# Optimization experiments

Measured on AMD Instinct MI355X. Metric: run time of the kernel, lower is better.

Reference implementation:

```python
import jax, jax.numpy as jnp
import numpy as np

D = 200            # embedding_dim == GRU hidden size
N_LABELS = 28000   # MeSH label count (graph nodes)
VOCAB = 50000
B = 4
T_AB = 384         # abstract length
T_TI = 64          # title length
N_EDGES = 224000   # ~8 edges per label node


def reverse_padded(x, lengths):
    # reverse the first lengths[b] timesteps of each padded sequence
    T = x.shape[1]
    t = jnp.arange(T)
    idx = jnp.where(t[None, :] < lengths[:, None], lengths[:, None] - 1 - t[None, :], t[None, :])
    return jnp.take_along_axis(x, idx[:, :, None], axis=1)


def gru_dir(x, lengths, wih, whh, bih, bhh, reverse):
    # PyTorch-semantics GRU over a padded batch (packed-sequence equivalent):
    # hidden state freezes past each sequence length; padded outputs are zero.
    Bb, T, _ = x.shape
    Hh = whh.shape[1]
    if reverse:
        x = reverse_padded(x, lengths)
    gx = jnp.einsum('bti,gi->btg', x, wih) + bih   # [B,T,3H], torch gate order r,z,n

    def step(h, inp):
        g_t, t = inp
        gh = h @ whh.T + bhh
        r = jax.nn.sigmoid(g_t[:, :Hh] + gh[:, :Hh])
        z = jax.nn.sigmoid(g_t[:, Hh:2 * Hh] + gh[:, Hh:2 * Hh])
        n = jnp.tanh(g_t[:, 2 * Hh:] + r * gh[:, 2 * Hh:])
        h_new = (1.0 - z) * n + z * h
        mask = (t < lengths)[:, None]
        h = jnp.where(mask, h_new, h)
        return h, jnp.where(mask, h_new, 0.0)

    h0 = jnp.zeros((Bb, Hh), x.dtype)
    _, outs = jax.lax.scan(step, h0, (jnp.swapaxes(gx, 0, 1), jnp.arange(T)))
    outs = jnp.swapaxes(outs, 0, 1)
    if reverse:
        outs = reverse_padded(outs, lengths)
    return outs


def forward_impl(input_abstract, input_title, ab_length, title_length, edge_src, edge_dst,
                 g_node_feature, emb,
                 wih_l0f, whh_l0f, bih_l0f, bhh_l0f, wih_l0b, whh_l0b, bih_l0b, bhh_l0b,
                 wih_l1f, whh_l1f, bih_l1f, bhh_l1f, wih_l1b, whh_l1b, bih_l1b, bhh_l1b,
                 gcn_w1, gcn_b1, gcn_w2, gcn_b2, fc1_w, fc1_b, fc2_w, fc2_b):
    # --- LabelNet: two GCN layers (copy_src message + sum reduce, then Linear) ---
    def gcn_layer(feat, W, b):
        agg = jax.ops.segment_sum(feat[edge_src], edge_dst, num_segments=N_LABELS)
        return agg @ W.T + b

    h = jax.nn.relu(gcn_layer(g_node_feature, gcn_w1, gcn_b1))
    lab = gcn_layer(h, gcn_w2, gcn_b2)
    label_feature = jnp.concatenate([lab, g_node_feature], axis=1)   # [N, 2D]

    gru_params = [
        (wih_l0f, whh_l0f, bih_l0f, bhh_l0f, wih_l0b, whh_l0b, bih_l0b, bhh_l0b),
        (wih_l1f, whh_l1f, bih_l1f, bhh_l1f, wih_l1b, whh_l1b, bih_l1b, bhh_l1b),
    ]

    def branch(tokens, lengths):
        x = emb[tokens]                                              # [B,T,D]
        for (wif, whf, bif, bhf, wib, whb, bib, bhb) in gru_params:
            f = gru_dir(x, lengths, wif, whf, bif, bhf, False)
            bwd = gru_dir(x, lengths, wib, whb, bib, bhb, True)
            x = jnp.concatenate([f, bwd], axis=-1)                   # [B,T,2D]
        # doc-label cross attention: softmax over the sequence dim (dim=1).
        # Padded positions output zero vectors -> logit 0, included in softmax
        # exactly as in the original torch code.
        atten = jax.nn.softmax(jnp.einsum('btd,nd->btn', x, label_feature), axis=1)
        return jnp.einsum('btd,btn->bnd', x, atten)                  # [B,N,2D]

    feat = branch(input_title, title_length) + branch(input_abstract, ab_length)
    y = jax.nn.leaky_relu(feat @ fc1_w.T + fc1_b, negative_slope=0.2)
    y = jax.nn.leaky_relu(y @ fc2_w.T + fc2_b, negative_slope=0.2)
    return y[..., 0]                                                 # [B, N]


def setup_inputs():
    key = jax.random.key(0)
    ks = jax.random.split(key, 32)
    it = iter(range(32))
    def nk():
        return ks[next(it)]
    s = 0.05
    inp = {}
    inp['input_abstract'] = jax.random.randint(nk(), (B, T_AB), 0, VOCAB)
    inp['input_title'] = jax.random.randint(nk(), (B, T_TI), 0, VOCAB)
    inp['ab_length'] = jax.random.randint(nk(), (B,), T_AB // 2, T_AB + 1).at[0].set(T_AB)
    inp['title_length'] = jax.random.randint(nk(), (B,), T_TI // 2, T_TI + 1).at[0].set(T_TI)
    inp['edge_src'] = jax.random.randint(nk(), (N_EDGES,), 0, N_LABELS)
    inp['edge_dst'] = jax.random.randint(nk(), (N_EDGES,), 0, N_LABELS)
    inp['g_node_feature'] = jax.random.normal(nk(), (N_LABELS, D)) * s
    inp['emb'] = jax.random.normal(nk(), (VOCAB, D)) * s
    for l in range(2):
        in_dim = D if l == 0 else 2 * D
        for d in ('f', 'b'):
            inp['wih_l%d%s' % (l, d)] = jax.random.normal(nk(), (3 * D, in_dim)) * s
            inp['whh_l%d%s' % (l, d)] = jax.random.normal(nk(), (3 * D, D)) * s
            inp['bih_l%d%s' % (l, d)] = jnp.zeros((3 * D,))
            inp['bhh_l%d%s' % (l, d)] = jnp.zeros((3 * D,))
    inp['gcn_w1'] = jax.random.normal(nk(), (D, D)) * s
    inp['gcn_b1'] = jnp.zeros((D,))
    inp['gcn_w2'] = jax.random.normal(nk(), (D, D)) * s
    inp['gcn_b2'] = jnp.zeros((D,))
    inp['fc1_w'] = jax.random.normal(nk(), (D, 2 * D)) * s
    inp['fc1_b'] = jnp.zeros((D,))
    inp['fc2_w'] = jax.random.normal(nk(), (1, D)) * s
    inp['fc2_b'] = jnp.zeros((1,))
    return inp


def reference(input_abstract, input_title, ab_length, title_length, edge_src, edge_dst,
              g_node_feature, emb,
              wih_l0f, whh_l0f, bih_l0f, bhh_l0f, wih_l0b, whh_l0b, bih_l0b, bhh_l0b,
              wih_l1f, whh_l1f, bih_l1f, bhh_l1f, wih_l1b, whh_l1b, bih_l1b, bhh_l1b,
              gcn_w1, gcn_b1, gcn_w2, gcn_b2, fc1_w, fc1_b, fc2_w, fc2_b):
    return forward_impl(input_abstract, input_title, ab_length, title_length, edge_src, edge_dst,
                        g_node_feature, emb,
                        wih_l0f, whh_l0f, bih_l0f, bhh_l0f, wih_l0b, whh_l0b, bih_l0b, bhh_l0b,
                        wih_l1f, whh_l1f, bih_l1f, bhh_l1f, wih_l1b, whh_l1b, bih_l1b, bhh_l1b,
                        gcn_w1, gcn_b1, gcn_w2, gcn_b2, fc1_w, fc1_b, fc2_w, fc2_b)
```

## Files before the change

### kernel.cpp

```cpp
#include <hip/hip_runtime.h>
#include <math.h>

#define NLAB 28000
#define NEDGE 224000
#define XFS 224

typedef _Float16 f16;
typedef _Float16 f16x8 __attribute__((ext_vector_type(8)));
typedef float f32x4 __attribute__((ext_vector_type(4)));


__device__ __forceinline__ void atomAddF(float* p, float v) {
  unsafeAtomicAdd(p, v);
}

struct RecurArgs {
  const float* gx[4];
  const float* wF[4];
  const float* bh[4];
  float* out[4];
  const int* len[4];
  int Tl[4];
  int dir[4];
};

#define COMPB(V, B) ((B) == 0 ? (V).x : (B) == 1 ? (V).y : (B) == 2 ? (V).z : (V).w)


__global__ void embed_gather(const int* __restrict__ tok, const float* __restrict__ emb,
                             float* __restrict__ x, int rows) {
  int idx = blockIdx.x * blockDim.x + threadIdx.x;
  if (idx >= rows * 50) return;
  int r = idx / 50, c = idx - r * 50;
  *(float4*)&x[(size_t)r * 200 + c * 4] =
      *(const float4*)&emb[(size_t)tok[r] * 200 + c * 4];
}


__global__ void pack_whhF(const float* __restrict__ whh, f16* __restrict__ out) {
  int e = blockIdx.x * 256 + threadIdx.x;
  if (e >= 40 * 7 * 512) return;
  int frag = e >> 9, r = e & 511;
  int l = r >> 3, j = r & 7;
  int mt = frag / 7, kt = frag - mt * 7;
  int m = mt * 16 + (l & 15);
  int k = kt * 32 + ((l >> 4) << 2) + (j & 3) + ((j >> 2) << 4);
  float v = (m < 600 && k < 200) ? whh[(size_t)m * 200 + k] : 0.f;
  f16 hi = (f16)v;
  out[e] = hi;
  out[40 * 7 * 512 + e] = (f16)((v - (float)hi) * 2048.f);
}


__global__ void gcn_gather(const float* __restrict__ feat, const int* __restrict__ src,
                           const int* __restrict__ dst, float* __restrict__ agg) {
  int wave = (int)((blockIdx.x * blockDim.x + threadIdx.x) >> 6);
  int lane = threadIdx.x & 63;
  if (wave >= NEDGE || lane >= 50) return;
  int s = src[wave], d = dst[wave];
  float4 v = *(const float4*)&feat[(size_t)s * 200 + lane * 4];
  float* p = &agg[(size_t)d * 200 + lane * 4];
  atomAddF(p + 0, v.x); atomAddF(p + 1, v.y);
  atomAddF(p + 2, v.z); atomAddF(p + 3, v.w);
}


template <int RELU, int BIAS>
__global__ __launch_bounds__(256, 2) void gemm_nt(
    const float* __restrict__ A, const float* __restrict__ Wt,
    const float* __restrict__ bias, float* __restrict__ C,
    int M, int N, int K, int ldc) {
  __shared__ float As[16][68];
  __shared__ float Bs[16][68];
  int tx = threadIdx.x & 15, ty = threadIdx.x >> 4;
  int m0 = blockIdx.y * 64, n0 = blockIdx.x * 64;
  float c[4][4] = {};
  int row = threadIdx.x >> 2;
  int kk = (threadIdx.x & 3) * 4;
  for (int k0 = 0; k0 < K; k0 += 16) {
    int gk = k0 + kk;
    float a0 = 0, a1 = 0, a2 = 0, a3 = 0;
    float b0 = 0, b1 = 0, b2 = 0, b3 = 0;
    int gm = m0 + row;
    if (gm < M) {
      if (gk + 3 < K) {
        float4 v = *(const float4*)&A[(size_t)gm * K + gk];
        a0 = v.x; a1 = v.y; a2 = v.z; a3 = v.w;
      } else {
        if (gk + 0 < K) a0 = A[(size_t)gm * K + gk + 0];
        if (gk + 1 < K) a1 = A[(size_t)gm * K + gk + 1];
        if (gk + 2 < K) a2 = A[(size_t)gm * K + gk + 2];
        if (gk + 3 < K) a3 = A[(size_t)gm * K + gk + 3];
      }
    }
    int gn = n0 + row;
    if (gn < N) {
      if (gk + 3 < K) {
        float4 v = *(const float4*)&Wt[(size_t)gn * K + gk];
        b0 = v.x; b1 = v.y; b2 = v.z; b3 = v.w;
      } else {
        if (gk + 0 < K) b0 = Wt[(size_t)gn * K + gk + 0];
        if (gk + 1 < K) b1 = Wt[(size_t)gn * K + gk + 1];
        if (gk + 2 < K) b2 = Wt[(size_t)gn * K + gk + 2];
        if (gk + 3 < K) b3 = Wt[(size_t)gn * K + gk + 3];
      }
    }
    As[kk + 0][row] = a0; As[kk + 1][row] = a1; As[kk + 2][row] = a2; As[kk + 3][row] = a3;
    Bs[kk + 0][row] = b0; Bs[kk + 1][row] = b1; Bs[kk + 2][row] = b2; Bs[kk + 3][row] = b3;
    __syncthreads();
#pragma unroll
    for (int k = 0; k < 16; k++) {
      float4 a4 = *(const float4*)&As[k][ty * 4];
      float4 b4 = *(const float4*)&Bs[k][tx * 4];
      c[0][0] = fmaf(a4.x, b4.x, c[0][0]); c[0][1] = fmaf(a4.x, b4.y, c[0][1]);
      c[0][2] = fmaf(a4.x, b4.z, c[0][2]); c[0][3] = fmaf(a4.x, b4.w, c[0][3]);
      c[1][0] = fmaf(a4.y, b4.x, c[1][0]); c[1][1] = fmaf(a4.y, b4.y, c[1][1]);
      c[1][2] = fmaf(a4.y, b4.z, c[1][2]); c[1][3] = fmaf(a4.y, b4.w, c[1][3]);
      c[2][0] = fmaf(a4.z, b4.x, c[2][0]); c[2][1] = fmaf(a4.z, b4.y, c[2][1]);
      c[2][2] = fmaf(a4.z, b4.z, c[2][2]); c[2][3] = fmaf(a4.z, b4.w, c[2][3]);
      c[3][0] = fmaf(a4.w, b4.x, c[3][0]); c[3][1] = fmaf(a4.w, b4.y, c[3][1]);
      c[3][2] = fmaf(a4.w, b4.z, c[3][2]); c[3][3] = fmaf(a4.w, b4.w, c[3][3]);
    }
    __syncthreads();
  }
#pragma unroll
  for (int i = 0; i < 4; i++) {
    int gm = m0 + ty * 4 + i;
    if (gm >= M) continue;
#pragma unroll
    for (int j = 0; j < 4; j++) {
      int gn = n0 + tx * 4 + j;
      if (gn >= N) continue;
      float v = c[i][j];
      if (BIAS) v += bias[gn];
      if (RELU) v = fmaxf(v, 0.f);
      C[(size_t)gm * ldc + gn] = v;
    }
  }
}


__global__ __launch_bounds__(512, 1) void gru_mfma(RecurArgs a) {
  int blk = blockIdx.x;
  const float* __restrict__ gx = a.gx[blk];
  const f16* __restrict__ whiP = (const f16*)a.wF[blk];
  const float* __restrict__ bh = a.bh[blk];
  float* __restrict__ outp = a.out[blk];
  const int* lenp = a.len[blk];
  int TT = a.Tl[blk];
  int bwd = a.dir[blk];
  int dirOff = bwd ? 200 : 0;

  __shared__ __align__(16) f16 wlds[16][7][512];
  __shared__ __align__(16) f16 hfrag[2][7][512];
  __shared__ float h[200][4];
  __shared__ float gh[600][4];
  __shared__ float bhs[600];
  __shared__ int lens[4];

  int tid = threadIdx.x, lane = tid & 63, w = tid >> 6;
  int l15 = lane & 15, lg = lane >> 4;

  for (int i = tid; i < 800; i += 512) ((float*)h)[i] = 0.f;
  for (int i = tid; i < 600; i += 512) bhs[i] = bh[i];
  for (int i = tid; i < 2 * 7 * 512; i += 512) ((f16*)hfrag)[i] = (f16)0.f;
  if (tid < 4) lens[tid] = lenp[tid];

#pragma unroll
  for (int i = 0; i < 2; i++)
#pragma unroll
    for (int kt = 0; kt < 7; kt++)
      *(f16x8*)&wlds[w * 2 + i][kt][lane * 8] =
          *(const f16x8*)(whiP + ((size_t)((w * 5 + i) * 7 + kt)) * 512 + lane * 8);
  __syncthreads();
  int maxlen = max(max(lens[0], lens[1]), max(lens[2], lens[3]));

  for (int s = 0; s < maxlen; s++) {
    float pgx[3][4];
    if (tid < 200) {
#pragma unroll
      for (int b = 0; b < 4; b++) {
        int Lb = lens[b];
        if (s < Lb) {
          int ta = bwd ? (Lb - 1 - s) : s;
          const float* gxr = gx + (size_t)(b * TT + ta) * 600;
          pgx[0][b] = gxr[tid];
          pgx[1][b] = gxr[200 + tid];
          pgx[2][b] = gxr[400 + tid];
        }
      }
    }
    f32x4 acc1[5], acc2[5];
#pragma unroll
    for (int i = 0; i < 5; i++) {
      acc1[i] = (f32x4){0.f, 0.f, 0.f, 0.f};
      acc2[i] = (f32x4){0.f, 0.f, 0.f, 0.f};
    }
#pragma unroll
    for (int kt = 0; kt < 7; kt++) {
      f16x8 hhi = *(const f16x8*)&hfrag[0][kt][lane * 8];
      f16x8 hlo = *(const f16x8*)&hfrag[1][kt][lane * 8];
#pragma unroll
      for (int i = 0; i < 5; i++) {
        const f16* base = whiP + ((size_t)((w * 5 + i) * 7 + kt)) * 512 + lane * 8;
        f16x8 whi = (i < 2) ? *(const f16x8*)&wlds[w * 2 + i][kt][lane * 8]
                            : *(const f16x8*)base;
        f16x8 wlo = *(const f16x8*)(base + (size_t)40 * 7 * 512);
        acc1[i] = __builtin_amdgcn_mfma_f32_16x16x32_f16(whi, hhi, acc1[i], 0, 0, 0);
        acc2[i] = __builtin_amdgcn_mfma_f32_16x16x32_f16(wlo, hhi, acc2[i], 0, 0, 0);
        acc2[i] = __builtin_amdgcn_mfma_f32_16x16x32_f16(whi, hlo, acc2[i], 0, 0, 0);
      }
    }
    if (l15 < 4) {
#pragma unroll
      for (int i = 0; i < 5; i++) {
        int mbase = (w * 5 + i) * 16 + lg * 4;
#pragma unroll
        for (int r = 0; r < 4; r++) {
          int m = mbase + r;
          if (m < 600) gh[m][l15] = acc1[i][r] + acc2[i][r] * (1.f / 2048.f);
        }
      }
    }
    __syncthreads();
    if (tid < 200) {
      int u = tid;
      float4 hold = *(const float4*)&h[u][0];
      float4 hnew = hold;
      float br = bhs[u], bz = bhs[200 + u], bn = bhs[400 + u];
#pragma unroll
      for (int b = 0; b < 4; b++) {
        int Lb = lens[b];
        if (s < Lb) {
          int ta = bwd ? (Lb - 1 - s) : s;
          float r = 1.f / (1.f + expf(-(pgx[0][b] + gh[u][b] + br)));
          float z = 1.f / (1.f + expf(-(pgx[1][b] + gh[200 + u][b] + bz)));
          float n = tanhf(pgx[2][b] + r * (gh[400 + u][b] + bn));
          float hn = (1.f - z) * n + z * COMPB(hold, b);
          if (b == 0) hnew.x = hn; else if (b == 1) hnew.y = hn;
          else if (b == 2) hnew.z = hn; else hnew.w = hn;
          outp[(size_t)(b * TT + ta) * 400 + dirOff + u] = hn;
        }
      }
      *(float4*)&h[u][0] = hnew;
      int kt = u >> 5;
      int lbase = ((u >> 2) & 3) << 4;
      int j = (u & 3) | (((u >> 4) & 1) << 2);
#pragma unroll
      for (int b = 0; b < 4; b++) {
        float hv = COMPB(hnew, b);
        f16 hi = (f16)hv;
        f16 lo = (f16)((hv - (float)hi) * 2048.f);
        hfrag[0][kt][(lbase + b) * 8 + j] = hi;
        hfrag[1][kt][(lbase + b) * 8 + j] = lo;
      }
    }
    __syncthreads();
  }
}


__global__ void cvt_lf_frags(const float* __restrict__ lab, const float* __restrict__ gnf,
                             f16* __restrict__ out) {
  int e = blockIdx.x * 256 + threadIdx.x;
  if (e >= 1752 * 13 * 512) return;
  int frag = e >> 9, r = e & 511;
  int l = r >> 3, j = r & 7;
  int nsub = frag / 13, kt = frag - nsub * 13;
  int label = nsub * 16 + (l & 15);
  int k = kt * 32 + ((l >> 4) << 2) + (j & 3) + ((j >> 2) << 4);
  float v = 0.f;
  if (label < NLAB && k < 400)
    v = (k < 200) ? lab[(size_t)label * 200 + k] : gnf[(size_t)label * 200 + k - 200];
  out[e] = (f16)v;
}

__global__ void cvt_x_frags(const float* __restrict__ x, f16* __restrict__ out, int TT) {
  int e = blockIdx.x * 256 + threadIdx.x;
  if (e >= 4 * TT * 13 * 512) return;
  int frag = e >> 9, r = e & 511;
  int l = r >> 3, j = r & 7;
  int kt = frag % 13, bt = frag / 13;
  int tt = bt % TT, b = bt / TT;
  int t = tt * 16 + (l & 15);
  int k = kt * 32 + ((l >> 4) << 2) + (j & 3) + ((j >> 2) << 4);
  float v = (k < 400) ? x[((size_t)b * TT * 16 + t) * 400 + k] : 0.f;
  out[e] = (f16)v;
}

__global__ void cvt_v_frags(const float* __restrict__ xf, f16* __restrict__ out, int KT) {
  int e = blockIdx.x * 256 + threadIdx.x;
  if (e >= 4 * KT * 13 * 2 * 512) return;
  int idx = e >> 9, r = e & 511;
  int l = r >> 3, j = r & 7;
  int hl = idx & 1, rest = idx >> 1;
  int dt = rest % 13, rest2 = rest / 13;
  int kt = rest2 % KT, b = rest2 / KT;
  int t = kt * 32 + ((l >> 4) << 2) + (j & 3) + ((j >> 2) << 4);
  int d = dt * 16 + (l & 15);
  float v = xf[((size_t)b * KT * 32 + t) * XFS + d];
  float hi = (float)(f16)v;
  out[e] = hl ? (f16)((v - hi) * 2048.f) : (f16)v;
}


__global__ __launch_bounds__(256, 2) void attn_mfma(
    const f16* __restrict__ lfF, const f16* __restrict__ xFab, const f16* __restrict__ xFti,
    const f16* __restrict__ vFab, const f16* __restrict__ vFti,
    const float* __restrict__ fc1b, const float* __restrict__ fc2w,
    const float* __restrict__ fc2b, float* __restrict__ outp) {
  __shared__ float SB[2][32][65];
  __shared__ float CRS[2][2][16];
  __shared__ float LIS[2][2][16];

  int tid = threadIdx.x, lane = tid & 63, w = tid >> 6;
  int nh = w >> 1, hl = w & 1;
  int b = blockIdx.y, nt = blockIdx.x;
  int l15 = lane & 15, lg = lane >> 4;

  f32x4 acc[2][13];
#pragma unroll
  for (int ns = 0; ns < 2; ns++)
#pragma unroll
    for (int dt = 0; dt < 13; dt++) acc[ns][dt] = (f32x4){0.f, 0.f, 0.f, 0.f};
  float mrun[4] = {-INFINITY, -INFINITY, -INFINITY, -INFINITY};
  float lrun[4] = {0.f, 0.f, 0.f, 0.f};

  for (int c = 0; c < 7; c++) {
    const bool ti = (c == 6);
    const f16* xb = ti ? xFti + (size_t)b * (4 * 13 * 512)
                       : xFab + ((size_t)(b * 24 + c * 4)) * 13 * 512;
    f32x4 S[2][2];
#pragma unroll
    for (int ns = 0; ns < 2; ns++)
#pragma unroll
      for (int ts = 0; ts < 2; ts++) S[ns][ts] = (f32x4){0.f, 0.f, 0.f, 0.f};
#pragma unroll
    for (int kh = 0; kh < 2; kh++) {
      const int kt0 = kh ? 7 : 0;
      const int ktn = kh ? 6 : 7;
      f16x8 la[2][7];
#pragma unroll
      for (int ns = 0; ns < 2; ns++) {
        const f16* lp = lfF + (((size_t)(nt * 4 + nh * 2 + ns)) * 13 + kt0) * 512 + lane * 8;
#pragma unroll
        for (int k = 0; k < 7; k++)
          if (k < ktn) la[ns][k] = *(const f16x8*)(lp + (size_t)k * 512);
      }
#pragma unroll
      for (int ts = 0; ts < 2; ts++) {
        const f16* xp = xb + (((size_t)(hl * 2 + ts)) * 13 + kt0) * 512 + lane * 8;
        f16x8 xa[7];
#pragma unroll
        for (int k = 0; k < 7; k++)
          if (k < ktn) xa[k] = *(const f16x8*)(xp + (size_t)k * 512);
#pragma unroll
        for (int ns = 0; ns < 2; ns++)
#pragma unroll
          for (int k = 0; k < 7; k++)
            if (k < ktn)
              S[ns][ts] = __builtin_amdgcn_mfma_f32_16x16x32_f16(la[ns][k], xa[k], S[ns][ts], 0, 0, 0);
      }
    }
    __syncthreads();
#pragma unroll
    for (int ns = 0; ns < 2; ns++)
#pragma unroll
      for (int ts = 0; ts < 2; ts++)
#pragma unroll
        for (int r = 0; r < 4; r++)
          SB[nh][ns * 16 + lg * 4 + r][(hl * 2 + ts) * 16 + l15] = S[ns][ts][r];
    __syncthreads();
    {
      float vv[4][4];
#pragma unroll
      for (int r = 0; r < 4; r++)
#pragma unroll
        for (int ts = 0; ts < 4; ts++)
          vv[r][ts] = SB[nh][hl * 16 + lg * 4 + r][ts * 16 + l15];
#pragma unroll
      for (int r = 0; r < 4; r++) {
        float tm = fmaxf(fmaxf(vv[r][0], vv[r][1]), fmaxf(vv[r][2], vv[r][3]));
        tm = fmaxf(tm, __shfl_xor(tm, 1));
        tm = fmaxf(tm, __shfl_xor(tm, 2));
        tm = fmaxf(tm, __shfl_xor(tm, 4));
        tm = fmaxf(tm, __shfl_xor(tm, 8));
        if (!ti) {
          float mn = fmaxf(mrun[r], tm);
          float cr = expf(mrun[r] - mn);
          float s = 0.f;
#pragma unroll
          for (int ts = 0; ts < 4; ts++) { vv[r][ts] = expf(vv[r][ts] - mn); s += vv[r][ts]; }
          s += __shfl_xor(s, 1); s += __shfl_xor(s, 2);
          s += __shfl_xor(s, 4); s += __shfl_xor(s, 8);
          lrun[r] = lrun[r] * cr + s;
          mrun[r] = mn;
#pragma unroll
          for (int ts = 0; ts < 4; ts++)
            SB[nh][hl * 16 + lg * 4 + r][ts * 16 + l15] = vv[r][ts];
          if (l15 == 0) {
            CRS[nh][hl][lg * 4 + r] = cr;
            if (c == 5) LIS[nh][hl][lg * 4 + r] = 1.f / lrun[r];
          }
        } else {
          float s = 0.f;
#pragma unroll
          for (int ts = 0; ts < 4; ts++) { vv[r][ts] = expf(vv[r][ts] - tm); s += vv[r][ts]; }
          s += __shfl_xor(s, 1); s += __shfl_xor(s, 2);
          s += __shfl_xor(s, 4); s += __shfl_xor(s, 8);
          float inv = 1.f / s;
#pragma unroll
          for (int ts = 0; ts < 4; ts++)
            SB[nh][hl * 16 + lg * 4 + r][ts * 16 + l15] = vv[r][ts] * inv;
        }
      }
    }
    __syncthreads();
    if (!ti) {
#pragma unroll
      for (int ns = 0; ns < 2; ns++)
#pragma unroll
        for (int r = 0; r < 4; r++) {
          float cr = CRS[nh][ns][lg * 4 + r];
#pragma unroll
          for (int dt = 0; dt < 13; dt++) acc[ns][dt][r] *= cr;
        }
    } else {
#pragma unroll
      for (int ns = 0; ns < 2; ns++)
#pragma unroll
        for (int r = 0; r < 4; r++) {
          float li = LIS[nh][ns][lg * 4 + r];
#pragma unroll
          for (int dt = 0; dt < 13; dt++) acc[ns][dt][r] *= li;
        }
    }
    f16x8 pf[2][2];
#pragma unroll
    for (int ns = 0; ns < 2; ns++)
#pragma unroll
      for (int kt = 0; kt < 2; kt++)
#pragma unroll
        for (int j = 0; j < 8; j++) {
          int col = kt * 32 + (lg << 2) + (j & 3) + ((j >> 2) << 4);
          pf[ns][kt][j] = (f16)SB[nh][ns * 16 + l15][col];
        }
#pragma unroll
    for (int dt = 0; dt < 13; dt++)
#pragma unroll
      for (int kt = 0; kt < 2; kt++) {
        const f16* vp = (ti ? vFti + (((size_t)((b * 2 + kt) * 13 + dt)) * 2 + hl) * 512
                            : vFab + (((size_t)((b * 12 + c * 2 + kt) * 13 + dt)) * 2 + hl) * 512)
                        + lane * 8;
        f16x8 vf = *(const f16x8*)vp;
#pragma unroll
        for (int ns = 0; ns < 2; ns++)
          acc[ns][dt] = __builtin_amdgcn_mfma_f32_16x16x32_f16(pf[ns][kt], vf, acc[ns][dt], 0, 0, 0);
      }
  }

  float part[2][4] = {{0.f, 0.f, 0.f, 0.f}, {0.f, 0.f, 0.f, 0.f}};
#pragma unroll
  for (int p = 0; p < 4; p++) {
    const int dt0 = p * 4;
    const int dtn = (p == 3) ? 1 : 4;
    __syncthreads();
    if (hl) {
#pragma unroll
      for (int ns = 0; ns < 2; ns++)
#pragma unroll
        for (int q = 0; q < 4; q++)
          if (q < dtn)
#pragma unroll
            for (int r = 0; r < 4; r++)
              SB[nh][ns * 16 + lg * 4 + r][q * 16 + l15] = acc[ns][dt0 + q][r];
    }
    __syncthreads();
    if (!hl) {
#pragma unroll
      for (int ns = 0; ns < 2; ns++)
#pragma unroll
        for (int q = 0; q < 4; q++)
          if (q < dtn)
#pragma unroll
            for (int r = 0; r < 4; r++) {
              int d = (dt0 + q) * 16 + l15;
              float y = acc[ns][dt0 + q][r] +
                        SB[nh][ns * 16 + lg * 4 + r][q * 16 + l15] * (1.f / 2048.f);
              if (d < 200) {
                y += fc1b[d];
                y = y >= 0.f ? y : 0.2f * y;
                part[ns][r] = fmaf(y, fc2w[d], part[ns][r]);
              }
            }
    }
  }
  if (!hl) {
#pragma unroll
    for (int ns = 0; ns < 2; ns++)
#pragma unroll
      for (int r = 0; r < 4; r++) {
        float s = part[ns][r];
        s += __shfl_xor(s, 1); s += __shfl_xor(s, 2);
        s += __shfl_xor(s, 4); s += __shfl_xor(s, 8);
        part[ns][r] = s;
      }
    if (l15 == 0) {
      float f2b = fc2b[0];
#pragma unroll
      for (int ns = 0; ns < 2; ns++)
#pragma unroll
        for (int r = 0; r < 4; r++) {
          int label = nt * 64 + nh * 32 + ns * 16 + lg * 4 + r;
          if (label < NLAB) {
            float y = part[ns][r] + f2b;
            y = y >= 0.f ? y : 0.2f * y;
            outp[(size_t)b * NLAB + label] = y;
          }
        }
    }
  }
}


extern "C" void kernel_launch(void* const* d_in, const int* in_sizes, int n_in,
                              void* d_out, int out_size, void* d_ws, size_t ws_size,
                              hipStream_t stream) {
  (void)in_sizes; (void)n_in; (void)out_size; (void)ws_size;
  const int* tok_ab = (const int*)d_in[0];
  const int* tok_ti = (const int*)d_in[1];
  const int* len_ab = (const int*)d_in[2];
  const int* len_ti = (const int*)d_in[3];
  const int* esrc = (const int*)d_in[4];
  const int* edst = (const int*)d_in[5];
  const float* gnf = (const float*)d_in[6];
  const float* emb = (const float*)d_in[7];
  const float* wih0f = (const float*)d_in[8],  *whh0f = (const float*)d_in[9];
  const float* bih0f = (const float*)d_in[10], *bhh0f = (const float*)d_in[11];
  const float* wih0b = (const float*)d_in[12], *whh0b = (const float*)d_in[13];
  const float* bih0b = (const float*)d_in[14], *bhh0b = (const float*)d_in[15];
  const float* wih1f = (const float*)d_in[16], *whh1f = (const float*)d_in[17];
  const float* bih1f = (const float*)d_in[18], *bhh1f = (const float*)d_in[19];
  const float* wih1b = (const float*)d_in[20], *whh1b = (const float*)d_in[21];
  const float* bih1b = (const float*)d_in[22], *bhh1b = (const float*)d_in[23];
  const float* gw1 = (const float*)d_in[24], *gb1 = (const float*)d_in[25];
  const float* gw2 = (const float*)d_in[26], *gb2 = (const float*)d_in[27];
  const float* fc1w = (const float*)d_in[28], *fc1b = (const float*)d_in[29];
  const float* fc2w = (const float*)d_in[30], *fc2b = (const float*)d_in[31];

  float* W = (float*)d_ws;
  float* agg  = W;
  float* hbuf = W + 5600000;
  float* lab  = W + 11200000;
  float* whhF0f = W;
  float* whhF0b = W + 143360;
  float* whhF1f = W + 286720;
  float* whhF1b = W + 430080;
  float* x0ab   = W + 480000;
  float* x0ti   = W + 787200;
  float* gxfab  = W + 838400;
  float* gxbab  = W + 1760000;
  float* gxfti  = W + 2681600;
  float* gxbti  = W + 2835200;
  float* out0ab = W + 2988800;
  float* out0ti = W + 3603200;
  float* out1ab = W + 3705600;
  float* out1ti = W + 4320000;
  float* xf1ab  = W + 4422400;
  float* xf1ti  = W + 4766464;
  f16* xFab = (f16*)(W + 838400);
  f16* xFti = (f16*)(W + 1157888);
  f16* vFab = (f16*)(W + 1211136);
  f16* vFti = (f16*)(W + 1530624);
  f16* lfF  = (f16*)(W + 4850000);

  int gatherBlocks = NEDGE / 4;
  dim3 gGcn(4, 438);

  hipMemsetAsync(agg, 0, 5600000 * sizeof(float), stream);
  gcn_gather<<<gatherBlocks, 256, 0, stream>>>(gnf, esrc, edst, agg);
  gemm_nt<1, 1><<<gGcn, 256, 0, stream>>>(agg, gw1, gb1, hbuf, NLAB, 200, 200, 200);
  hipMemsetAsync(agg, 0, 5600000 * sizeof(float), stream);
  gcn_gather<<<gatherBlocks, 256, 0, stream>>>(hbuf, esrc, edst, agg);
  gemm_nt<0, 1><<<gGcn, 256, 0, stream>>>(agg, gw2, gb2, lab, NLAB, 200, 200, 200);

  cvt_lf_frags<<<(1752 * 13 * 512 + 255) / 256, 256, 0, stream>>>(lab, gnf, lfF);

  embed_gather<<<(1536 * 50 + 255) / 256, 256, 0, stream>>>(tok_ab, emb, x0ab, 1536);
  embed_gather<<<(256 * 50 + 255) / 256, 256, 0, stream>>>(tok_ti, emb, x0ti, 256);
  hipMemsetAsync(out0ab, 0, (size_t)1433600 * sizeof(float), stream);
  hipMemsetAsync(xf1ab, 0, (size_t)(344064 + 57344) * sizeof(float), stream);

  dim3 gGxAb(10, 24), gGxTi(10, 4);
  gemm_nt<0, 1><<<gGxAb, 256, 0, stream>>>(x0ab, wih0f, bih0f, gxfab, 1536, 600, 200, 600);
  gemm_nt<0, 1><<<gGxAb, 256, 0, stream>>>(x0ab, wih0b, bih0b, gxbab, 1536, 600, 200, 600);
  gemm_nt<0, 1><<<gGxTi, 256, 0, stream>>>(x0ti, wih0f, bih0f, gxfti, 256, 600, 200, 600);
  gemm_nt<0, 1><<<gGxTi, 256, 0, stream>>>(x0ti, wih0b, bih0b, gxbti, 256, 600, 200, 600);

  int packN = (40 * 7 * 512 + 255) / 256;
  pack_whhF<<<packN, 256, 0, stream>>>(whh0f, (f16*)whhF0f);
  pack_whhF<<<packN, 256, 0, stream>>>(whh0b, (f16*)whhF0b);
  pack_whhF<<<packN, 256, 0, stream>>>(whh1f, (f16*)whhF1f);
  pack_whhF<<<packN, 256, 0, stream>>>(whh1b, (f16*)whhF1b);

  RecurArgs r0;
  r0.gx[0] = gxfab; r0.gx[1] = gxbab; r0.gx[2] = gxfti; r0.gx[3] = gxbti;
  r0.wF[0] = whhF0f; r0.wF[1] = whhF0b; r0.wF[2] = whhF0f; r0.wF[3] = whhF0b;
  r0.bh[0] = bhh0f; r0.bh[1] = bhh0b; r0.bh[2] = bhh0f; r0.bh[3] = bhh0b;
  r0.out[0] = out0ab; r0.out[1] = out0ab; r0.out[2] = out0ti; r0.out[3] = out0ti;
  r0.len[0] = len_ab; r0.len[1] = len_ab; r0.len[2] = len_ti; r0.len[3] = len_ti;
  r0.Tl[0] = 384; r0.Tl[1] = 384; r0.Tl[2] = 64; r0.Tl[3] = 64;
  r0.dir[0] = 0; r0.dir[1] = 1; r0.dir[2] = 0; r0.dir[3] = 1;
  gru_mfma<<<4, 512, 0, stream>>>(r0);

  gemm_nt<0, 1><<<gGxAb, 256, 0, stream>>>(out0ab, wih1f, bih1f, gxfab, 1536, 600, 400, 600);
  gemm_nt<0, 1><<<gGxAb, 256, 0, stream>>>(out0ab, wih1b, bih1b, gxbab, 1536, 600, 400, 600);
  gemm_nt<0, 1><<<gGxTi, 256, 0, stream>>>(out0ti, wih1f, bih1f, gxfti, 256, 600, 400, 600);
  gemm_nt<0, 1><<<gGxTi, 256, 0, stream>>>(out0ti, wih1b, bih1b, gxbti, 256, 600, 400, 600);

  RecurArgs r1 = r0;
  r1.wF[0] = whhF1f; r1.wF[1] = whhF1b;
  r1.wF[2] = whhF1f; r1.wF[3] = whhF1b;
  r1.bh[0] = bhh1f; r1.bh[1] = bhh1b; r1.bh[2] = bhh1f; r1.bh[3] = bhh1b;
  r1.out[0] = out1ab; r1.out[1] = out1ab; r1.out[2] = out1ti; r1.out[3] = out1ti;
  gru_mfma<<<4, 512, 0, stream>>>(r1);

  gemm_nt<0, 0><<<dim3(4, 24), 256, 0, stream>>>(out1ab, fc1w, nullptr, xf1ab, 1536, 200, 400, XFS);
  gemm_nt<0, 0><<<dim3(4, 4), 256, 0, stream>>>(out1ti, fc1w, nullptr, xf1ti, 256, 200, 400, XFS);

  cvt_x_frags<<<(4 * 24 * 13 * 512 + 255) / 256, 256, 0, stream>>>(out1ab, xFab, 24);
  cvt_x_frags<<<(4 * 4 * 13 * 512 + 255) / 256, 256, 0, stream>>>(out1ti, xFti, 4);
  cvt_v_frags<<<(4 * 12 * 13 * 2 * 512 + 255) / 256, 256, 0, stream>>>(xf1ab, vFab, 12);
  cvt_v_frags<<<(4 * 2 * 13 * 2 * 512 + 255) / 256, 256, 0, stream>>>(xf1ti, vFti, 2);

  attn_mfma<<<dim3(438, 4), 256, 0, stream>>>(
      lfF, xFab, xFti, vFab, vFti, fc1b, fc2w, fc2b, (float*)d_out);
}
```

Measured before the change: 6.273 ms.

## Overlap GCN edge-gather atomics with GRU recurrence in one fused launch

The GRU recurrence launches only 4 blocks and leaves most CUs idle, so the GCN scatter-add is folded into the same launch. Blocks 0-3 run the GRU and the other 248 blocks walk the edge list with a grid-stride loop, doing atomic adds into the aggregation buffer. The first GCN layer's gather rides along with GRU layer 0 and the second with GRU layer 1. The follow-up GEMMs are moved after each launch, and the workspace is re-laid out so the GCN buffers no longer alias GRU buffers. The cost is possible memory and atomic contention slowing the latency-critical GRU blocks.

```diff
diff --git a/kernel.cpp b/kernel.cpp
--- a/kernel.cpp
+++ b/kernel.cpp
@@ -49,19 +49,6 @@
   f16 hi = (f16)v;
   out[e] = hi;
   out[40 * 7 * 512 + e] = (f16)((v - (float)hi) * 2048.f);
-}
-
-
-__global__ void gcn_gather(const float* __restrict__ feat, const int* __restrict__ src,
-                           const int* __restrict__ dst, float* __restrict__ agg) {
-  int wave = (int)((blockIdx.x * blockDim.x + threadIdx.x) >> 6);
-  int lane = threadIdx.x & 63;
-  if (wave >= NEDGE || lane >= 50) return;
-  int s = src[wave], d = dst[wave];
-  float4 v = *(const float4*)&feat[(size_t)s * 200 + lane * 4];
-  float* p = &agg[(size_t)d * 200 + lane * 4];
-  atomAddF(p + 0, v.x); atomAddF(p + 1, v.y);
-  atomAddF(p + 2, v.z); atomAddF(p + 3, v.w);
 }
 
 
@@ -140,7 +127,31 @@
 }
 
 
-__global__ __launch_bounds__(512, 1) void gru_mfma(RecurArgs a) {
+__global__ __launch_bounds__(512, 1) void gru_fused(RecurArgs a,
+    const float* __restrict__ gfeat, const int* __restrict__ esrc,
+    const int* __restrict__ edst, float* __restrict__ gagg) {
+  __shared__ __align__(16) f16 wlds[16][7][512];
+  __shared__ __align__(16) f16 hfrag[2][7][512];
+  __shared__ float h[200][4];
+  __shared__ float gh[600][4];
+  __shared__ float bhs[600];
+  __shared__ int lens[4];
+
+  if (blockIdx.x >= 4) {
+    int lane = threadIdx.x & 63;
+    if (lane >= 50) return;
+    int nb = gridDim.x - 4;
+    int wav = (blockIdx.x - 4) * 8 + (threadIdx.x >> 6);
+    for (int e = wav; e < NEDGE; e += nb * 8) {
+      int s = esrc[e], d = edst[e];
+      float4 v = *(const float4*)&gfeat[(size_t)s * 200 + lane * 4];
+      float* p = &gagg[(size_t)d * 200 + lane * 4];
+      atomAddF(p + 0, v.x); atomAddF(p + 1, v.y);
+      atomAddF(p + 2, v.z); atomAddF(p + 3, v.w);
+    }
+    return;
+  }
+
   int blk = blockIdx.x;
   const float* __restrict__ gx = a.gx[blk];
   const f16* __restrict__ whiP = (const f16*)a.wF[blk];
@@ -150,13 +161,6 @@
   int TT = a.Tl[blk];
   int bwd = a.dir[blk];
   int dirOff = bwd ? 200 : 0;
-
-  __shared__ __align__(16) f16 wlds[16][7][512];
-  __shared__ __align__(16) f16 hfrag[2][7][512];
-  __shared__ float h[200][4];
-  __shared__ float gh[600][4];
-  __shared__ float bhs[600];
-  __shared__ int lens[4];
 
   int tid = threadIdx.x, lane = tid & 63, w = tid >> 6;
   int l15 = lane & 15, lg = lane >> 4;
@@ -550,58 +554,47 @@
 
   float* W = (float*)d_ws;
   float* agg  = W;
-  float* hbuf = W + 5600000;
-  float* lab  = W + 11200000;
-  float* whhF0f = W;
-  float* whhF0b = W + 143360;
-  float* whhF1f = W + 286720;
-  float* whhF1b = W + 430080;
-  float* x0ab   = W + 480000;
-  float* x0ti   = W + 787200;
-  float* gxfab  = W + 838400;
-  float* gxbab  = W + 1760000;
-  float* gxfti  = W + 2681600;
-  float* gxbti  = W + 2835200;
-  float* out0ab = W + 2988800;
-  float* out0ti = W + 3603200;
-  float* out1ab = W + 3705600;
-  float* out1ti = W + 4320000;
-  float* xf1ab  = W + 4422400;
-  float* xf1ti  = W + 4766464;
-  f16* xFab = (f16*)(W + 838400);
-  f16* xFti = (f16*)(W + 1157888);
-  f16* vFab = (f16*)(W + 1211136);
-  f16* vFti = (f16*)(W + 1530624);
-  f16* lfF  = (f16*)(W + 4850000);
-
-  int gatherBlocks = NEDGE / 4;
+  f16*   lfF  = (f16*)W;
+  float* hbuf = W + 5830656;
+  float* lab  = W + 5830656;
+  float* x0ab   = W + 11200000;
+  float* x0ti   = W + 11507200;
+  float* whhF0f = W + 11558400;
+  float* whhF0b = W + 11701760;
+  float* whhF1f = W + 11845120;
+  float* whhF1b = W + 11988480;
+  float* gxfab  = W + 12131840;
+  float* gxbab  = W + 13053440;
+  float* gxfti  = W + 13975040;
+  float* gxbti  = W + 14128640;
+  float* out0ab = W + 14282240;
+  float* out0ti = W + 14896640;
+  float* out1ab = W + 14999040;
+  float* out1ti = W + 15613440;
+  float* xf1ab  = W + 15715840;
+  float* xf1ti  = W + 16059904;
+  f16* xFab = (f16*)(W + 12131840);
+  f16* xFti = (f16*)(W + 12451328);
+  f16* vFab = (f16*)(W + 12504576);
+  f16* vFti = (f16*)(W + 12824064);
+
   dim3 gGcn(4, 438);
-
-  hipMemsetAsync(agg, 0, 5600000 * sizeof(float), stream);
-  gcn_gather<<<gatherBlocks, 256, 0, stream>>>(gnf, esrc, edst, agg);
-  gemm_nt<1, 1><<<gGcn, 256, 0, stream>>>(agg, gw1, gb1, hbuf, NLAB, 200, 200, 200);
-  hipMemsetAsync(agg, 0, 5600000 * sizeof(float), stream);
-  gcn_gather<<<gatherBlocks, 256, 0, stream>>>(hbuf, esrc, edst, agg);
-  gemm_nt<0, 1><<<gGcn, 256, 0, stream>>>(agg, gw2, gb2, lab, NLAB, 200, 200, 200);
-
-  cvt_lf_frags<<<(1752 * 13 * 512 + 255) / 256, 256, 0, stream>>>(lab, gnf, lfF);
+  dim3 gGxAb(10, 24), gGxTi(10, 4);
+  int packN = (40 * 7 * 512 + 255) / 256;
 
   embed_gather<<<(1536 * 50 + 255) / 256, 256, 0, stream>>>(tok_ab, emb, x0ab, 1536);
   embed_gather<<<(256 * 50 + 255) / 256, 256, 0, stream>>>(tok_ti, emb, x0ti, 256);
-  hipMemsetAsync(out0ab, 0, (size_t)1433600 * sizeof(float), stream);
-  hipMemsetAsync(xf1ab, 0, (size_t)(344064 + 57344) * sizeof(float), stream);
-
-  dim3 gGxAb(10, 24), gGxTi(10, 4);
+  pack_whhF<<<packN, 256, 0, stream>>>(whh0f, (f16*)whhF0f);
+  pack_whhF<<<packN, 256, 0, stream>>>(whh0b, (f16*)whhF0b);
+  pack_whhF<<<packN, 256, 0, stream>>>(whh1f, (f16*)whhF1f);
+  pack_whhF<<<packN, 256, 0, stream>>>(whh1b, (f16*)whhF1b);
+  hipMemsetAsync(out0ab, 0, (size_t)1835008 * sizeof(float), stream);
+
   gemm_nt<0, 1><<<gGxAb, 256, 0, stream>>>(x0ab, wih0f, bih0f, gxfab, 1536, 600, 200, 600);
   gemm_nt<0, 1><<<gGxAb, 256, 0, stream>>>(x0ab, wih0b, bih0b, gxbab, 1536, 600, 200, 600);
   gemm_nt<0, 1><<<gGxTi, 256, 0, stream>>>(x0ti, wih0f, bih0f, gxfti, 256, 600, 200, 600);
   gemm_nt<0, 1><<<gGxTi, 256, 0, stream>>>(x0ti, wih0b, bih0b, gxbti, 256, 600, 200, 600);
-
-  int packN = (40 * 7 * 512 + 255) / 256;
-  pack_whhF<<<packN, 256, 0, stream>>>(whh0f, (f16*)whhF0f);
-  pack_whhF<<<packN, 256, 0, stream>>>(whh0b, (f16*)whhF0b);
-  pack_whhF<<<packN, 256, 0, stream>>>(whh1f, (f16*)whhF1f);
-  pack_whhF<<<packN, 256, 0, stream>>>(whh1b, (f16*)whhF1b);
+  hipMemsetAsync(agg, 0, 5600000 * sizeof(float), stream);
 
   RecurArgs r0;
   r0.gx[0] = gxfab; r0.gx[1] = gxbab; r0.gx[2] = gxfti; r0.gx[3] = gxbti;
@@ -611,8 +604,10 @@
   r0.len[0] = len_ab; r0.len[1] = len_ab; r0.len[2] = len_ti; r0.len[3] = len_ti;
   r0.Tl[0] = 384; r0.Tl[1] = 384; r0.Tl[2] = 64; r0.Tl[3] = 64;
   r0.dir[0] = 0; r0.dir[1] = 1; r0.dir[2] = 0; r0.dir[3] = 1;
-  gru_mfma<<<4, 512, 0, stream>>>(r0);
-
+  gru_fused<<<252, 512, 0, stream>>>(r0, gnf, esrc, edst, agg);
+
+  gemm_nt<1, 1><<<gGcn, 256, 0, stream>>>(agg, gw1, gb1, hbuf, NLAB, 200, 200, 200);
+  hipMemsetAsync(agg, 0, 5600000 * sizeof(float), stream);
   gemm_nt<0, 1><<<gGxAb, 256, 0, stream>>>(out0ab, wih1f, bih1f, gxfab, 1536, 600, 400, 600);
   gemm_nt<0, 1><<<gGxAb, 256, 0, stream>>>(out0ab, wih1b, bih1b, gxbab, 1536, 600, 400, 600);
   gemm_nt<0, 1><<<gGxTi, 256, 0, stream>>>(out0ti, wih1f, bih1f, gxfti, 256, 600, 400, 600);
@@ -623,7 +618,10 @@
   r1.wF[2] = whhF1f; r1.wF[3] = whhF1b;
   r1.bh[0] = bhh1f; r1.bh[1] = bhh1b; r1.bh[2] = bhh1f; r1.bh[3] = bhh1b;
   r1.out[0] = out1ab; r1.out[1] = out1ab; r1.out[2] = out1ti; r1.out[3] = out1ti;
-  gru_mfma<<<4, 512, 0, stream>>>(r1);
+  gru_fused<<<252, 512, 0, stream>>>(r1, hbuf, esrc, edst, agg);
+
+  gemm_nt<0, 1><<<gGcn, 256, 0, stream>>>(agg, gw2, gb2, lab, NLAB, 200, 200, 200);
+  cvt_lf_frags<<<(1752 * 13 * 512 + 255) / 256, 256, 0, stream>>>(lab, gnf, lfF);
 
   gemm_nt<0, 0><<<dim3(4, 24), 256, 0, stream>>>(out1ab, fc1w, nullptr, xf1ab, 1536, 200, 400, XFS);
   gemm_nt<0, 0><<<dim3(4, 4), 256, 0, stream>>>(out1ti, fc1w, nullptr, xf1ti, 256, 200, 400, XFS);
```

Result: faster. 5.891 ms (-6.1%).
